# Performance work log

Measured on AMD Instinct MI355X. Metric: run time of the kernel, lower is better.

The kernel has to match this reference:

```python
import jax, jax.numpy as jnp
import numpy as np

# SLAYER SRM-ALPHA neuron / simulation constants (from netParams)
THETA = 10.0      # spike threshold
TAU_SR = 10.0     # PSP (SRM) time constant
TAU_REF = 1.0     # refractory time constant
SCALE_REF = 2.0
TAU_RHO = 1.0     # surrogate-gradient width (unused in fwd)
SCALE_RHO = 1.0
TS = 1.0
K_SRM = 100       # truncation of alpha kernel (values < 1e-4 beyond this)
K_REF = 16

def _alpha_kernel(tau, K, mult):
    t = jnp.arange(K, dtype=jnp.float32) * TS
    return mult * (t / tau) * jnp.exp(1.0 - t / tau)

SRM_KERNEL = _alpha_kernel(TAU_SR, K_SRM, 1.0)                       # eps(t)
REF_KERNEL = _alpha_kernel(TAU_REF, K_REF, -2.0 * THETA * SCALE_REF)  # nu(t)

def heaviside(u):
    return (u >= THETA).astype(u.dtype)

def psp(x):
    # causal temporal convolution with SRM alpha kernel; x: (..., T)
    T = x.shape[-1]
    K = SRM_KERNEL.shape[0]
    flat = x.reshape(-1, 1, T)  # (N, C=1, T)
    out = jax.lax.conv_general_dilated(flat, SRM_KERNEL[::-1].reshape(1, 1, K),
                                       (1,), [(K - 1, 0)])
    return out.reshape(x.shape)

def spike(v):
    # SLAYER spike generation with refractory feedback; v: (..., T)
    refk = REF_KERNEL[1:]          # refractory affects strictly future steps
    L = refk.shape[0]
    vT = jnp.moveaxis(v, -1, 0)    # (T, ...)
    pend0 = jnp.zeros(vT.shape[1:] + (L,), v.dtype)  # pending refractory contributions
    def step(pend, vt):
        u = vt + pend[..., 0]
        s = heaviside(u)
        pend = jnp.concatenate([pend[..., 1:], jnp.zeros_like(pend[..., :1])], axis=-1) \
               + s[..., None] * refk
        return pend, s
    _, sT = jax.lax.scan(step, pend0, vT)
    return jnp.moveaxis(sT, 0, -1)

def conv_t(x, W, pad):
    # per-timestep 2D conv (slayer.conv uses Conv3d with kernel (k,k,1), no bias)
    B, C, H, Wd, T = x.shape
    xt = jnp.transpose(x, (0, 4, 1, 2, 3)).reshape(B * T, C, H, Wd)
    y = jax.lax.conv_general_dilated(xt, W, (1, 1), [(pad, pad), (pad, pad)])
    Co, Ho, Wo = y.shape[1:]
    return jnp.transpose(y.reshape(B, T, Co, Ho, Wo), (0, 2, 3, 4, 1))

def pool_t(x):
    # slayer.pool(2): 2x2 sum-pool with constant weight 1.1*theta per element
    s = jax.lax.reduce_window(x, 0.0, jax.lax.add, (1, 1, 2, 2, 1), (1, 1, 2, 2, 1), 'VALID')
    return s * (1.1 * THETA)

def _forward(spikeInput, W1, W2, W3, W4, Wfc):
    x = spike(conv_t(psp(spikeInput), W1, 1))   # (B,16,48,48,T)
    x = spike(pool_t(psp(x)))                   # (B,16,24,24,T)
    x = spike(conv_t(psp(x), W2, 1))            # (B,32,24,24,T)
    x = spike(pool_t(psp(x)))                   # (B,32,12,12,T)
    x = spike(conv_t(psp(x), W3, 1))            # (B,64,12,12,T)
    x = spike(pool_t(psp(x)))                   # (B,64,6,6,T)
    x = spike(conv_t(psp(x), W4, 1))            # (B,64,6,6,T)
    x = spike(jnp.einsum('bchwt,kchw->bkt', psp(x), Wfc))  # (B,10,T)
    return x

def setup_inputs():
    key = jax.random.key(0)
    ks = jax.random.split(key, 6)
    B, T = 4, 200
    spikeInput = (jax.random.uniform(ks[0], (B, 2, 50, 50, T)) < 0.05).astype(jnp.float32)
    W1 = 0.5 * jax.random.normal(ks[1], (16, 2, 5, 5), jnp.float32)
    W2 = 0.25 * jax.random.normal(ks[2], (32, 16, 3, 3), jnp.float32)
    W3 = 0.25 * jax.random.normal(ks[3], (64, 32, 3, 3), jnp.float32)
    W4 = 0.25 * jax.random.normal(ks[4], (64, 64, 3, 3), jnp.float32)
    Wfc = 0.1 * jax.random.normal(ks[5], (10, 64, 6, 6), jnp.float32)
    return {"spikeInput": spikeInput, "W1": W1, "W2": W2, "W3": W3, "W4": W4, "Wfc": Wfc}

def reference(spikeInput, W1, W2, W3, W4, Wfc):
    return _forward(spikeInput, W1, W2, W3, W4, Wfc)
```

## Files before the change

### kernel.cpp

```cpp
#include <hip/hip_runtime.h>
#include <math.h>


#define THETA 10.0f
#define RSTRIDE 204

__global__ void prep_kernel(const float* __restrict__ W1, const float* __restrict__ W2,
                            const float* __restrict__ W3, const float* __restrict__ W4,
                            float* HQ, float* rk,
                            float* wt1, float* wt2, float* wt3, float* wt4) {
    int i = blockIdx.x * 256 + threadIdx.x;
    if (i < 144) {
        int k = i - 15;
        float val = 0.0f;
        if (k >= 0 && k <= 99) {
            float tf = (float)k;
            float x = tf / 10.0f;
            val = x * (float)exp((double)(1.0f - x));
        }
        HQ[i] = val;
    } else if (i < 160) {
        int j = i - 144;
        if (j < 15) {
            float t = (float)(j + 1);
            rk[j] = (-40.0f * t) * (float)exp((double)(1.0f - t));
        }
    } else if (i < 960) {
        int j = i - 160, co = j / 50, tp = j % 50;
        wt1[tp * 16 + co] = W1[j];
    } else if (i < 5568) {
        int j = i - 960, co = j / 144, tp = j % 144;
        wt2[tp * 32 + co] = W2[j];
    } else if (i < 24000) {
        int j = i - 5568, co = j / 288, tp = j % 288;
        wt3[tp * 64 + co] = W3[j];
    } else if (i < 60864) {
        int j = i - 24000, co = j / 576, tp = j % 576;
        wt4[tp * 64 + co] = W4[j];
    }
}

#define FIR_STEP(A0, A1, A2, A3, qx, qy, qz, qw, hA, hB)  \
    A0 = fmaf(hA.x, qw, A0);                              \
    A1 = fmaf(hA.y, qw, A1);                              \
    A2 = fmaf(hA.z, qw, A2);                              \
    A3 = fmaf(hA.w, qw, A3);                              \
    A0 = fmaf(hA.y, qz, A0);                              \
    A1 = fmaf(hA.z, qz, A1);                              \
    A2 = fmaf(hA.w, qz, A2);                              \
    A3 = fmaf(hB.x, qz, A3);                              \
    A0 = fmaf(hA.z, qy, A0);                              \
    A1 = fmaf(hA.w, qy, A1);                              \
    A2 = fmaf(hB.x, qy, A2);                              \
    A3 = fmaf(hB.y, qy, A3);                              \
    A0 = fmaf(hA.w, qx, A0);                              \
    A1 = fmaf(hB.x, qx, A1);                              \
    A2 = fmaf(hB.y, qx, A2);                              \
    A3 = fmaf(hB.z, qx, A3);

#define SCAN4(XV, p, rk)                                          \
    {                                                             \
        float u_, sv_;                                            \
        u_ = XV.x + p[0]; sv_ = (u_ >= THETA) ? 1.0f : 0.0f;      \
        XV.x = sv_;                                               \
        _Pragma("unroll")                                         \
        for (int i_ = 0; i_ < 14; ++i_) p[i_] = fmaf(sv_, rk[i_], p[i_ + 1]); \
        p[14] = sv_ * rk[14];                                     \
        u_ = XV.y + p[0]; sv_ = (u_ >= THETA) ? 1.0f : 0.0f;      \
        XV.y = sv_;                                               \
        _Pragma("unroll")                                         \
        for (int i_ = 0; i_ < 14; ++i_) p[i_] = fmaf(sv_, rk[i_], p[i_ + 1]); \
        p[14] = sv_ * rk[14];                                     \
        u_ = XV.z + p[0]; sv_ = (u_ >= THETA) ? 1.0f : 0.0f;      \
        XV.z = sv_;                                               \
        _Pragma("unroll")                                         \
        for (int i_ = 0; i_ < 14; ++i_) p[i_] = fmaf(sv_, rk[i_], p[i_ + 1]); \
        p[14] = sv_ * rk[14];                                     \
        u_ = XV.w + p[0]; sv_ = (u_ >= THETA) ? 1.0f : 0.0f;      \
        XV.w = sv_;                                               \
        _Pragma("unroll")                                         \
        for (int i_ = 0; i_ < 14; ++i_) p[i_] = fmaf(sv_, rk[i_], p[i_ + 1]); \
        p[14] = sv_ * rk[14];                                     \
    }

template <int NSUB>
__device__ __forceinline__ void fir_run(const float* __restrict__ row,
                                        const float4* __restrict__ HQ4,
                                        int t0, int jend, float4 (&acc)[NSUB]) {
    float4 H[5];
    #pragma unroll
    for (int m = 0; m < 5; ++m) H[m] = HQ4[m];
    const float* bp = row + t0 + 4 * (NSUB - 1);
    for (int j = 0; j <= jend; ++j) {
        const float4 qv = *reinterpret_cast<const float4*>(bp);
        const float4 Hn = HQ4[j + 5];
        #pragma unroll
        for (int d = 0; d < NSUB; ++d) {
            const float4 hA = H[d + 4 - NSUB];
            const float4 hB = H[d + 5 - NSUB];
            FIR_STEP(acc[d].x, acc[d].y, acc[d].z, acc[d].w,
                     qv.x, qv.y, qv.z, qv.w, hA, hB)
        }
        #pragma unroll
        for (int m = 0; m < 4; ++m) H[m] = H[m + 1];
        H[4] = Hn;
        bp -= 4;
    }
}

template <bool SCAN>
__global__ __launch_bounds__(512) void spikepsp_kernel(const float* __restrict__ in,
                                                       float* __restrict__ out,
                                                       const float* __restrict__ HQ,
                                                       const float* __restrict__ rkt,
                                                       int n) {
    __shared__ __align__(16) float tile[64 * RSTRIDE];
    const int l = threadIdx.x & 63;
    const int w = threadIdx.x >> 6;
    const int s0 = blockIdx.x * 64;
    for (int i = threadIdx.x; i < 3200; i += 512) {
        const int slot = i / 50, q = i - slot * 50;
        const int ser = s0 + slot;
        float4 v = make_float4(0.f, 0.f, 0.f, 0.f);
        if (ser < n) v = *reinterpret_cast<const float4*>(in + (long)ser * 200 + 4 * q);
        *reinterpret_cast<float4*>(&tile[slot * RSTRIDE + 4 * q]) = v;
    }
    __syncthreads();
    if (SCAN) {
        if (w == 0) {
            float rk[15];
            #pragma unroll
            for (int i = 0; i < 15; ++i) rk[i] = rkt[i];
            float p[15];
            #pragma unroll
            for (int i = 0; i < 15; ++i) p[i] = 0.0f;
            float* row = tile + l * RSTRIDE;
            for (int tq = 0; tq < 50; ++tq) {
                float4 xv = *reinterpret_cast<const float4*>(&row[4 * tq]);
                SCAN4(xv, p, rk)
                *reinterpret_cast<float4*>(&row[4 * tq]) = xv;
            }
        }
        __syncthreads();
    }
    const bool valid = (s0 + l) < n;
    const float* row = tile + l * RSTRIDE;
    const float4* HQ4 = reinterpret_cast<const float4*>(HQ);
    float* op = out + (long)(s0 + l) * 200;
    for (int item = w; item < 13; item += 8) {
        if (item < 12) {
            const int t0 = 16 * item;
            const int gm = (4 * item < 25) ? 4 * item : 25;
            float4 acc[4];
            #pragma unroll
            for (int d = 0; d < 4; ++d) acc[d] = make_float4(0.f, 0.f, 0.f, 0.f);
            fir_run<4>(row, HQ4, t0, gm + 3, acc);
            if (valid) {
                #pragma unroll
                for (int d = 0; d < 4; ++d)
                    *reinterpret_cast<float4*>(op + t0 + 4 * d) = acc[d];
            }
        } else {
            float4 acc[2];
            #pragma unroll
            for (int d = 0; d < 2; ++d) acc[d] = make_float4(0.f, 0.f, 0.f, 0.f);
            fir_run<2>(row, HQ4, 192, 26, acc);
            if (valid) {
                #pragma unroll
                for (int d = 0; d < 2; ++d)
                    *reinterpret_cast<float4*>(op + 192 + 4 * d) = acc[d];
            }
        }
    }
}

__global__ __launch_bounds__(512) void spikepsppool_kernel(const float* __restrict__ in,
                                                           float* __restrict__ out,
                                                           const float* __restrict__ HQ,
                                                           const float* __restrict__ rkt,
                                                           int C, int HO, int WO) {
    __shared__ __align__(16) float tile[64 * RSTRIDE];
    __shared__ int sbase[64];
    const int l = threadIdx.x & 63;
    const int w = threadIdx.x >> 6;
    const int o0 = blockIdx.x * 16;
    const int H = 2 * HO, W = 2 * WO;
    if (threadIdx.x < 64) {
        const int oi = threadIdx.x >> 2, p = threadIdx.x & 3;
        const int o = o0 + oi;
        const int wo = o % WO; int tmp = o / WO;
        const int ho = tmp % HO; tmp /= HO;
        const int c = tmp % C; const int b = tmp / C;
        sbase[threadIdx.x] = ((b * C + c) * H + 2 * ho + (p >> 1)) * W + 2 * wo + (p & 1);
    }
    __syncthreads();
    for (int i = threadIdx.x; i < 3200; i += 512) {
        const int slot = i / 50, q = i - slot * 50;
        const float4 v = *reinterpret_cast<const float4*>(in + (long)sbase[slot] * 200 + 4 * q);
        *reinterpret_cast<float4*>(&tile[slot * RSTRIDE + 4 * q]) = v;
    }
    __syncthreads();
    if (w == 0) {
        float rk[15];
        #pragma unroll
        for (int i = 0; i < 15; ++i) rk[i] = rkt[i];
        float p[15];
        #pragma unroll
        for (int i = 0; i < 15; ++i) p[i] = 0.0f;
        float* row = tile + l * RSTRIDE;
        for (int tq = 0; tq < 50; ++tq) {
            float4 xv = *reinterpret_cast<const float4*>(&row[4 * tq]);
            SCAN4(xv, p, rk)
            *reinterpret_cast<float4*>(&row[4 * tq]) = xv;
        }
    }
    __syncthreads();
    const int qb = l & ~3;
    const float* row = tile + l * RSTRIDE;
    const float4* HQ4 = reinterpret_cast<const float4*>(HQ);
    float* op = out + (long)(o0 + (l >> 2)) * 200;
    auto qsum = [&](float v) -> float {
        const float v0 = __shfl(v, qb + 0);
        const float v1 = __shfl(v, qb + 1);
        const float v2 = __shfl(v, qb + 2);
        const float v3 = __shfl(v, qb + 3);
        return (((v0 + v1) + v2) + v3) * 11.0f;
    };
    for (int item = w; item < 13; item += 8) {
        if (item < 12) {
            const int t0 = 16 * item;
            const int gm = (4 * item < 25) ? 4 * item : 25;
            float4 acc[4];
            #pragma unroll
            for (int d = 0; d < 4; ++d) acc[d] = make_float4(0.f, 0.f, 0.f, 0.f);
            fir_run<4>(row, HQ4, t0, gm + 3, acc);
            #pragma unroll
            for (int d = 0; d < 4; ++d) {
                float4 r;
                r.x = qsum(acc[d].x); r.y = qsum(acc[d].y);
                r.z = qsum(acc[d].z); r.w = qsum(acc[d].w);
                if ((l & 3) == 0)
                    *reinterpret_cast<float4*>(op + t0 + 4 * d) = r;
            }
        } else {
            float4 acc[2];
            #pragma unroll
            for (int d = 0; d < 2; ++d) acc[d] = make_float4(0.f, 0.f, 0.f, 0.f);
            fir_run<2>(row, HQ4, 192, 26, acc);
            #pragma unroll
            for (int d = 0; d < 2; ++d) {
                float4 r;
                r.x = qsum(acc[d].x); r.y = qsum(acc[d].y);
                r.z = qsum(acc[d].z); r.w = qsum(acc[d].w);
                if ((l & 3) == 0)
                    *reinterpret_cast<float4*>(op + 192 + 4 * d) = r;
            }
        }
    }
}

template <int K, int PAD, int CI, int COG>
__global__ __launch_bounds__(256) void conv_kernel(const float* __restrict__ x,
                                                   const float* __restrict__ wt,
                                                   float* __restrict__ out,
                                                   int Co, int H, int W,
                                                   int HO, int WO) {
    const int l = threadIdx.x & 63;
    const int wv = threadIdx.x >> 6;
    if (l >= 50) return;
    const int p = blockIdx.x * 4 + wv;
    const int wo = p % WO, ho = p / WO;
    const int co0 = blockIdx.y * COG;
    const int b = blockIdx.z;
    const int t0 = l * 4;
    float4 acc[COG];
    #pragma unroll
    for (int c = 0; c < COG; ++c) acc[c] = make_float4(0.f, 0.f, 0.f, 0.f);
    const float* xb = x + ((long)b * CI * H * W) * 200 + t0;
    for (int ci = 0; ci < CI; ++ci) {
        #pragma unroll
        for (int kh = 0; kh < K; ++kh) {
            const int hi = ho + kh - PAD;
            if (hi < 0 || hi >= H) continue;
            #pragma unroll
            for (int kw = 0; kw < K; ++kw) {
                const int wi = wo + kw - PAD;
                if (wi < 0 || wi >= W) continue;
                const float4 v = *reinterpret_cast<const float4*>(
                    xb + ((long)(ci * H + hi) * W + wi) * 200);
                const float* wp = wt + ((ci * K + kh) * K + kw) * Co + co0;
                #pragma unroll
                for (int c = 0; c < COG; ++c) {
                    const float wv_ = wp[c];
                    acc[c].x = fmaf(wv_, v.x, acc[c].x);
                    acc[c].y = fmaf(wv_, v.y, acc[c].y);
                    acc[c].z = fmaf(wv_, v.z, acc[c].z);
                    acc[c].w = fmaf(wv_, v.w, acc[c].w);
                }
            }
        }
    }
    const long hwN = (long)HO * WO;
    const long ob = ((long)(b * Co + co0) * HO + ho) * WO + wo;
    #pragma unroll
    for (int c = 0; c < COG; ++c)
        *reinterpret_cast<float4*>(out + (ob + c * hwN) * 200 + t0) = acc[c];
}

template <int CI, int COG>
__global__ __launch_bounds__(256) void conv3_kernel(const float* __restrict__ x,
                                                    const float* __restrict__ wt,
                                                    float* __restrict__ out,
                                                    int Co, int H, int W) {
    const int l = threadIdx.x & 63;
    const int wv = threadIdx.x >> 6;
    if (l >= 50) return;
    const int p = blockIdx.x * 4 + wv;
    const int wo = p % W, ho = p / W;
    const int co0 = blockIdx.y * COG;
    const int b = blockIdx.z;
    const int t0 = l * 4;
    float4 acc[COG];
    #pragma unroll
    for (int c = 0; c < COG; ++c) acc[c] = make_float4(0.f, 0.f, 0.f, 0.f);

    bool vm[9];
    #pragma unroll
    for (int i = 0; i < 9; ++i) {
        const int hi = ho + i / 3 - 1, wi = wo + i % 3 - 1;
        vm[i] = (hi >= 0) && (hi < H) && (wi >= 0) && (wi < W);
    }
    const long cis = (long)H * W * 200;
    const float* pb = x + (long)b * CI * cis + ((long)(ho - 1) * W + (wo - 1)) * 200 + t0;

    float4 bufA[9], bufB[9];
    auto ld = [&](int ci, float4 (&B)[9]) {
        const float* pc = pb + ci * cis;
        #pragma unroll
        for (int i = 0; i < 9; ++i) {
            B[i] = vm[i] ? *reinterpret_cast<const float4*>(pc + ((i / 3) * W + (i % 3)) * 200)
                         : make_float4(0.f, 0.f, 0.f, 0.f);
        }
    };
    auto fm = [&](const float4 (&B)[9], int ci) {
        #pragma unroll
        for (int i = 0; i < 9; ++i) {
            const float* wp = wt + (ci * 9 + i) * Co + co0;
            #pragma unroll
            for (int c = 0; c < COG; ++c) {
                const float wv_ = wp[c];
                acc[c].x = fmaf(wv_, B[i].x, acc[c].x);
                acc[c].y = fmaf(wv_, B[i].y, acc[c].y);
                acc[c].z = fmaf(wv_, B[i].z, acc[c].z);
                acc[c].w = fmaf(wv_, B[i].w, acc[c].w);
            }
        }
    };

    ld(0, bufA);
    #pragma unroll 1
    for (int ci = 0; ci < CI; ci += 2) {
        ld(ci + 1, bufB);
        fm(bufA, ci);
        if (ci + 2 < CI) ld(ci + 2, bufA);
        fm(bufB, ci + 1);
    }

    const long hwN = (long)H * W;
    const long ob = ((long)(b * Co + co0) * H + ho) * W + wo;
    #pragma unroll
    for (int c = 0; c < COG; ++c)
        *reinterpret_cast<float4*>(out + (ob + c * hwN) * 200 + t0) = acc[c];
}

__global__ __launch_bounds__(256) void spike_kernel(const float* __restrict__ v,
                                                    float* __restrict__ s,
                                                    const float* __restrict__ rkt,
                                                    int n) {
    const int nid = blockIdx.x * 256 + threadIdx.x;
    if (nid >= n) return;
    float rk[15];
    #pragma unroll
    for (int i = 0; i < 15; ++i) rk[i] = rkt[i];
    float p[15];
    #pragma unroll
    for (int i = 0; i < 15; ++i) p[i] = 0.0f;
    const float* vp = v + (long)nid * 200;
    float* sp = s + (long)nid * 200;
    for (int t = 0; t < 200; ++t) {
        const float u = vp[t] + p[0];
        const float sv = (u >= THETA) ? 1.0f : 0.0f;
        sp[t] = sv;
        #pragma unroll
        for (int i = 0; i < 14; ++i) p[i] = fmaf(sv, rk[i], p[i + 1]);
        p[14] = sv * rk[14];
    }
}

__global__ __launch_bounds__(64) void fc_kernel(const float* __restrict__ x,
                                                const float* __restrict__ wf,
                                                float* __restrict__ out) {
    const int k = blockIdx.x, b = blockIdx.y, l = threadIdx.x;
    if (l >= 25) return;
    const int t0 = blockIdx.z * 100 + l * 4;
    float4 acc = make_float4(0.f, 0.f, 0.f, 0.f);
    for (int c = 0; c < 64; ++c)
        #pragma unroll
        for (int h = 0; h < 6; ++h)
            #pragma unroll
            for (int w = 0; w < 6; ++w) {
                const float4 v = *reinterpret_cast<const float4*>(
                    x + (((long)(b * 64 + c) * 6 + h) * 6 + w) * 200 + t0);
                const float wv_ = wf[((k * 64 + c) * 6 + h) * 6 + w];
                acc.x = fmaf(wv_, v.x, acc.x);
                acc.y = fmaf(wv_, v.y, acc.y);
                acc.z = fmaf(wv_, v.z, acc.z);
                acc.w = fmaf(wv_, v.w, acc.w);
            }
    *reinterpret_cast<float4*>(out + ((long)b * 10 + k) * 200 + t0) = acc;
}

extern "C" void kernel_launch(void* const* d_in, const int* in_sizes, int n_in,
                              void* d_out, int out_size, void* d_ws, size_t ws_size,
                              hipStream_t stream) {
    const float* x_in = (const float*)d_in[0];
    const float* W1 = (const float*)d_in[1];
    const float* W2 = (const float*)d_in[2];
    const float* W3 = (const float*)d_in[3];
    const float* W4 = (const float*)d_in[4];
    const float* Wfc = (const float*)d_in[5];
    float* outp = (float*)d_out;

    float* ws = (float*)d_ws;
    float* HQ  = ws;
    float* rk  = ws + 144;
    float* wt1 = ws + 160;
    float* wt2 = wt1 + 800;
    float* wt3 = wt2 + 4608;
    float* wt4 = wt3 + 18432;
    float* A   = wt4 + 36864;
    float* B   = A + 7372800;
    float* C   = B + 29491200;

    hipLaunchKernelGGL(prep_kernel, dim3(238), dim3(256), 0, stream,
                       W1, W2, W3, W4, HQ, rk, wt1, wt2, wt3, wt4);

    hipLaunchKernelGGL((spikepsp_kernel<false>), dim3(313), dim3(512), 0, stream,
                       x_in, A, HQ, rk, 20000);
    hipLaunchKernelGGL((conv_kernel<5, 1, 2, 16>), dim3(2304 / 4, 1, 4), dim3(256), 0, stream,
                       A, wt1, B, 16, 50, 50, 48, 48);
    hipLaunchKernelGGL(spikepsppool_kernel, dim3(36864 / 16), dim3(512), 0, stream,
                       B, A, HQ, rk, 16, 24, 24);
    hipLaunchKernelGGL((spikepsp_kernel<true>), dim3(36864 / 64), dim3(512), 0, stream,
                       A, B, HQ, rk, 36864);
    hipLaunchKernelGGL((conv3_kernel<16, 8>), dim3(576 / 4, 4, 4), dim3(256), 0, stream,
                       B, wt2, C, 32, 24, 24);
    hipLaunchKernelGGL(spikepsppool_kernel, dim3(18432 / 16), dim3(512), 0, stream,
                       C, A, HQ, rk, 32, 12, 12);
    hipLaunchKernelGGL((spikepsp_kernel<true>), dim3(18432 / 64), dim3(512), 0, stream,
                       A, B, HQ, rk, 18432);
    hipLaunchKernelGGL((conv3_kernel<32, 8>), dim3(144 / 4, 8, 4), dim3(256), 0, stream,
                       B, wt3, C, 64, 12, 12);
    hipLaunchKernelGGL(spikepsppool_kernel, dim3(9216 / 16), dim3(512), 0, stream,
                       C, A, HQ, rk, 64, 6, 6);
    hipLaunchKernelGGL((spikepsp_kernel<true>), dim3(9216 / 64), dim3(512), 0, stream,
                       A, B, HQ, rk, 9216);
    hipLaunchKernelGGL((conv3_kernel<64, 4>), dim3(36 / 4, 16, 4), dim3(256), 0, stream,
                       B, wt4, C, 64, 6, 6);
    hipLaunchKernelGGL((spikepsp_kernel<true>), dim3(9216 / 64), dim3(512), 0, stream,
                       C, B, HQ, rk, 9216);
    hipLaunchKernelGGL(fc_kernel, dim3(10, 4, 2), dim3(64), 0, stream, B, Wfc, A);
    hipLaunchKernelGGL(spike_kernel, dim3(1), dim3(256), 0, stream, A, outp, rk, 40);
    (void)in_sizes; (void)n_in; (void)out_size; (void)ws_size;
}
```

Measured before the change: 730.9 us.

## Restructure FC kernel to stage time-slice inputs in shared memory across outputs

The fully connected layer is remapped so each block handles one batch and an 8-timestep slice, stages all 2304 input features for that slice into LDS, and computes all 10 output neurons from the shared copy. Before, each of 80 blocks re-read the whole input slab from global memory for a single output neuron. The new version reads the input once per batch and time slice and launches 100 blocks. It uses 72KB of shared memory per block, and only 20 of 64 threads do the long serial 2304-step reduction, which limits parallelism.

```diff
diff --git a/kernel.cpp b/kernel.cpp
--- a/kernel.cpp
+++ b/kernel.cpp
@@ -400,24 +400,32 @@
 __global__ __launch_bounds__(64) void fc_kernel(const float* __restrict__ x,
                                                 const float* __restrict__ wf,
                                                 float* __restrict__ out) {
-    const int k = blockIdx.x, b = blockIdx.y, l = threadIdx.x;
-    if (l >= 25) return;
-    const int t0 = blockIdx.z * 100 + l * 4;
-    float4 acc = make_float4(0.f, 0.f, 0.f, 0.f);
-    for (int c = 0; c < 64; ++c)
-        #pragma unroll
-        for (int h = 0; h < 6; ++h)
-            #pragma unroll
-            for (int w = 0; w < 6; ++w) {
-                const float4 v = *reinterpret_cast<const float4*>(
-                    x + (((long)(b * 64 + c) * 6 + h) * 6 + w) * 200 + t0);
-                const float wv_ = wf[((k * 64 + c) * 6 + h) * 6 + w];
-                acc.x = fmaf(wv_, v.x, acc.x);
-                acc.y = fmaf(wv_, v.y, acc.y);
-                acc.z = fmaf(wv_, v.z, acc.z);
-                acc.w = fmaf(wv_, v.w, acc.w);
-            }
-    *reinterpret_cast<float4*>(out + ((long)b * 10 + k) * 200 + t0) = acc;
+    __shared__ __align__(16) float xs[2304 * 8];
+    const int b = blockIdx.x;
+    const int t0 = blockIdx.y * 8;
+    const int l = threadIdx.x;
+    const float* xb = x + (long)b * 2304 * 200 + t0;
+    for (int i = l; i < 4608; i += 64) {
+        const int m = i >> 1, q = i & 1;
+        const float4 v = *reinterpret_cast<const float4*>(xb + (long)m * 200 + 4 * q);
+        *reinterpret_cast<float4*>(&xs[m * 8 + 4 * q]) = v;
+    }
+    __syncthreads();
+    if (l < 20) {
+        const int k = l >> 1, q = l & 1;
+        float4 acc = make_float4(0.f, 0.f, 0.f, 0.f);
+        const float* wp = wf + k * 2304;
+        const float* xp = xs + 4 * q;
+        for (int m = 0; m < 2304; ++m) {
+            const float4 v = *reinterpret_cast<const float4*>(xp + m * 8);
+            const float wv_ = wp[m];
+            acc.x = fmaf(wv_, v.x, acc.x);
+            acc.y = fmaf(wv_, v.y, acc.y);
+            acc.z = fmaf(wv_, v.z, acc.z);
+            acc.w = fmaf(wv_, v.w, acc.w);
+        }
+        *reinterpret_cast<float4*>(out + ((long)b * 10 + k) * 200 + t0 + 4 * q) = acc;
+    }
 }
 
 extern "C" void kernel_launch(void* const* d_in, const int* in_sizes, int n_in,
@@ -469,7 +477,7 @@
                        B, wt4, C, 64, 6, 6);
     hipLaunchKernelGGL((spikepsp_kernel<true>), dim3(9216 / 64), dim3(512), 0, stream,
                        C, B, HQ, rk, 9216);
-    hipLaunchKernelGGL(fc_kernel, dim3(10, 4, 2), dim3(64), 0, stream, B, Wfc, A);
+    hipLaunchKernelGGL(fc_kernel, dim3(4, 25), dim3(64), 0, stream, B, Wfc, A);
     hipLaunchKernelGGL(spike_kernel, dim3(1), dim3(256), 0, stream, A, outp, rk, 40);
     (void)in_sizes; (void)n_in; (void)out_size; (void)ws_size;
 }
```

Result: faster. 705.6 us (-3.5%).
